# Kernel optimization log

Measured on AMD Instinct MI355X. Metric: run time of the kernel, lower is better.

The kernel has to match this reference:

```python
import jax, jax.numpy as jnp
import numpy as np

NUM_GROUPS = 32
EPS = 1e-05
HT_MIN = -1.0
HT_MAX = 1.0


def setup_inputs() -> dict:
    key = jax.random.key(0)
    k1, k2, k3 = jax.random.split(key, 3)
    B, IN, OUT = 4096, 2048, 2048
    x = jax.random.normal(k1, (B, IN), dtype=jnp.float32)
    # kaiming-uniform-ish scale for weight, uniform bias bound 1/sqrt(in)
    weight = jax.random.normal(k2, (OUT, IN), dtype=jnp.float32) * (1.0 / np.sqrt(IN))
    bias = jax.random.uniform(k3, (OUT,), dtype=jnp.float32, minval=-1.0 / np.sqrt(IN), maxval=1.0 / np.sqrt(IN))
    gn_weight = jnp.ones((OUT,), dtype=jnp.float32)
    gn_bias = jnp.zeros((OUT,), dtype=jnp.float32)
    return {"x": x, "weight": weight, "bias": bias, "gn_weight": gn_weight, "gn_bias": gn_bias}


def reference(x, weight, bias, gn_weight, gn_bias):
    # Linear: y = x @ W^T + b   -> [B, OUT]
    y = jnp.einsum("bi,oi->bo", x, weight) + bias
    B, C = y.shape
    G = NUM_GROUPS
    yg = y.reshape(B, G, C // G)
    mean = jnp.mean(yg, axis=-1, keepdims=True)
    var = jnp.mean(jnp.square(yg), axis=-1, keepdims=True) - jnp.square(mean)
    yn = ((yg - mean) * jax.lax.rsqrt(var + EPS)).reshape(B, C)
    out = yn * gn_weight + gn_bias
    return jnp.clip(out, HT_MIN, HT_MAX)
```

## Files before the change

### kernel.cpp

```cpp
#include <hip/hip_runtime.h>
#include <stdint.h>

#define B_ROWS 4096
#define C_OUT  2048
#define C_IN   2048
#define EPS    1e-5f

typedef __attribute__((ext_vector_type(8))) short bf16x8;
typedef __attribute__((ext_vector_type(4))) float f32x4;

__device__ __forceinline__ unsigned short f2bf(float f) {
    uint32_t u = __float_as_uint(f);
    uint32_t r = (u + 0x7fffu + ((u >> 16) & 1u)) >> 16;
    return (unsigned short)r;
}

__global__ void cvt_f32_bf16_kernel(const float* __restrict__ x,
                                    const float* __restrict__ w,
                                    unsigned short* __restrict__ xb,
                                    unsigned short* __restrict__ wb,
                                    int nx4, int nw4) {
    int i = blockIdx.x * blockDim.x + threadIdx.x;
    const float* src;
    unsigned short* dst;
    if (i < nx4) {
        src = x; dst = xb;
    } else {
        i -= nx4;
        if (i >= nw4) return;
        src = w; dst = wb;
    }
    float4 v = ((const float4*)src)[i];
    ushort4 o;
    o.x = f2bf(v.x); o.y = f2bf(v.y); o.z = f2bf(v.z); o.w = f2bf(v.w);
    ((ushort4*)dst)[i] = o;
}

__global__ __launch_bounds__(512, 2)
void gemm_gn_kernel(const unsigned short* __restrict__ A,
                    const unsigned short* __restrict__ W,
                    const float* __restrict__ bias,
                    const float* __restrict__ gnw,
                    const float* __restrict__ gnb,
                    float* __restrict__ out) {
    __shared__ __align__(16) unsigned short smem[3 * 24576];

    const int bc   = blockIdx.x;
    const int br   = blockIdx.y;
    const int tid  = threadIdx.x;
    const int lane = tid & 63;
    const int wave = tid >> 6;
    const int wr   = wave >> 1;
    const int wc   = wave & 1;
    const int c16  = lane & 15;
    const int quad = lane >> 4;

    f32x4 acc[4][4];
#pragma unroll
    for (int i = 0; i < 4; i++)
#pragma unroll
        for (int j = 0; j < 4; j++) acc[i][j] = (f32x4){0.f, 0.f, 0.f, 0.f};

    const int r0 = tid >> 3;
    const int qo = ((tid & 7) ^ (r0 & 7)) * 8;
    const unsigned short* gA = A + (size_t)(br * 256 + r0) * C_IN + qo;
    const unsigned short* gB = W + (size_t)(bc * 128 + r0) * C_IN + qo;
    const int t8 = tid * 8;

#define STAGE_H(dst, k0, half)                                                                      \
    do {                                                                                            \
        _Pragma("unroll")                                                                           \
        for (int n = (half) * 2; n < (half) * 2 + 2; n++)                                           \
            __builtin_amdgcn_global_load_lds(                                                       \
                (const __attribute__((address_space(1))) void*)(gA + (size_t)(n * 64) * C_IN + (k0)), \
                (__attribute__((address_space(3))) void*)((dst) + n * 4096 + t8), 16, 0, 0);        \
        __builtin_amdgcn_global_load_lds(                                                           \
            (const __attribute__((address_space(1))) void*)(gB + (size_t)((half) * 64) * C_IN + (k0)), \
            (__attribute__((address_space(3))) void*)((dst) + 16384 + (half) * 4096 + t8), 16, 0, 0); \
    } while (0)

    unsigned short* bf0 = smem;
    unsigned short* bf1 = smem + 24576;
    unsigned short* bf2 = smem + 49152;

    const int qs0 = (quad ^ (c16 & 7)) * 8;
    const int qs1 = ((4 + quad) ^ (c16 & 7)) * 8;
    int offA[4], offB[4];
#pragma unroll
    for (int i = 0; i < 4; i++) offA[i] = (wr * 64 + i * 16 + c16) * 64;
#pragma unroll
    for (int j = 0; j < 4; j++) offB[j] = 16384 + (wc * 64 + j * 16 + c16) * 64;

    STAGE_H(bf0, 0, 0);  STAGE_H(bf0, 0, 1);
    STAGE_H(bf1, 64, 0); STAGE_H(bf1, 64, 1);
    asm volatile("s_waitcnt vmcnt(6)" ::: "memory");
    __builtin_amdgcn_s_barrier();

    const unsigned short* pr = bf0;
    const unsigned short* pn = bf1;
    unsigned short*       ps = bf2;

    bf16x8 a0[4], b0[4], a1[4], b1[4];
#pragma unroll
    for (int i = 0; i < 4; i++) a0[i] = *(const bf16x8*)(pr + offA[i] + qs0);
#pragma unroll
    for (int j = 0; j < 4; j++) b0[j] = *(const bf16x8*)(pr + offB[j] + qs0);

#pragma unroll 1
    for (int kt = 0; kt < 32; ++kt) {
        const int k2 = (kt + 2) * 64;

#pragma unroll
        for (int i = 0; i < 4; i++) a1[i] = *(const bf16x8*)(pr + offA[i] + qs1);
#pragma unroll
        for (int j = 0; j < 4; j++) b1[j] = *(const bf16x8*)(pr + offB[j] + qs1);
        if (kt < 30) STAGE_H(ps, k2, 0);
        asm volatile("s_waitcnt lgkmcnt(8)" ::: "memory");
        __builtin_amdgcn_sched_barrier(0);
        __builtin_amdgcn_s_setprio(1);
#pragma unroll
        for (int i = 0; i < 4; i++)
#pragma unroll
            for (int j = 0; j < 4; j++)
                acc[i][j] = __builtin_amdgcn_mfma_f32_16x16x32_bf16(a0[i], b0[j], acc[i][j], 0, 0, 0);
        __builtin_amdgcn_s_setprio(0);

        if (kt < 30)       asm volatile("s_waitcnt vmcnt(3)" ::: "memory");
        else if (kt == 30) asm volatile("s_waitcnt vmcnt(0)" ::: "memory");
        if (kt < 31) {
            __builtin_amdgcn_s_barrier();
#pragma unroll
            for (int i = 0; i < 4; i++) a0[i] = *(const bf16x8*)(pn + offA[i] + qs0);
#pragma unroll
            for (int j = 0; j < 4; j++) b0[j] = *(const bf16x8*)(pn + offB[j] + qs0);
            if (kt < 30) STAGE_H(ps, k2, 1);
            asm volatile("s_waitcnt lgkmcnt(8)" ::: "memory");
        } else {
            asm volatile("s_waitcnt lgkmcnt(0)" ::: "memory");
        }
        __builtin_amdgcn_sched_barrier(0);
        __builtin_amdgcn_s_setprio(1);
#pragma unroll
        for (int i = 0; i < 4; i++)
#pragma unroll
            for (int j = 0; j < 4; j++)
                acc[i][j] = __builtin_amdgcn_mfma_f32_16x16x32_bf16(a1[i], b1[j], acc[i][j], 0, 0, 0);
        __builtin_amdgcn_s_setprio(0);
        if (kt < 31) __builtin_amdgcn_s_barrier();

        const unsigned short* tmp = pr;
        pr = pn;
        pn = ps;
        ps = (unsigned short*)tmp;
    }

    const int colbase = bc * 128 + wc * 64;
    const int rowbase = br * 256 + wr * 64;
    float bv[4], gw[4], gb[4];
#pragma unroll
    for (int j = 0; j < 4; j++) {
        int col = colbase + j * 16 + c16;
        bv[j] = bias[col];
        gw[j] = gnw[col];
        gb[j] = gnb[col];
    }
#pragma unroll
    for (int i = 0; i < 4; i++) {
#pragma unroll
        for (int r = 0; r < 4; r++) {
            float s = 0.f, ss = 0.f;
#pragma unroll
            for (int j = 0; j < 4; j++) {
                float v = acc[i][j][r] + bv[j];
                acc[i][j][r] = v;
                s += v;
                ss += v * v;
            }
#pragma unroll
            for (int m = 1; m < 16; m <<= 1) {
                s  += __shfl_xor(s, m, 64);
                ss += __shfl_xor(ss, m, 64);
            }
            float mean = s * (1.f / 64.f);
            float var  = ss * (1.f / 64.f) - mean * mean;
            float rstd = rsqrtf(var + EPS);
            int row = rowbase + i * 16 + quad * 4 + r;
            float* orow = out + (size_t)row * C_OUT;
#pragma unroll
            for (int j = 0; j < 4; j++) {
                float v = (acc[i][j][r] - mean) * rstd * gw[j] + gb[j];
                v = fminf(1.f, fmaxf(-1.f, v));
                orow[colbase + j * 16 + c16] = v;
            }
        }
    }
}

extern "C" void kernel_launch(void* const* d_in, const int* in_sizes, int n_in,
                              void* d_out, int out_size, void* d_ws, size_t ws_size,
                              hipStream_t stream) {
    const float* x    = (const float*)d_in[0];
    const float* w    = (const float*)d_in[1];
    const float* bias = (const float*)d_in[2];
    const float* gnw  = (const float*)d_in[3];
    const float* gnb  = (const float*)d_in[4];
    float* out = (float*)d_out;

    unsigned short* xb = (unsigned short*)d_ws;
    unsigned short* wb = xb + (size_t)B_ROWS * C_IN;

    const int nx4 = B_ROWS * C_IN / 4;
    const int nw4 = C_OUT * C_IN / 4;
    cvt_f32_bf16_kernel<<<(nx4 + nw4 + 255) / 256, 256, 0, stream>>>(x, w, xb, wb, nx4, nw4);

    dim3 grid(C_OUT / 128, B_ROWS / 256);
    gemm_gn_kernel<<<grid, 512, 0, stream>>>(xb, wb, bias, gnw, gnb, out);
}
```

Baseline: 136.9 us.

## Load A fragments directly to registers, stage only W in LDS, remap blocks to XCDs

```diff
diff --git a/kernel.cpp b/kernel.cpp
--- a/kernel.cpp
+++ b/kernel.cpp
@@ -43,10 +43,14 @@
                     const float* __restrict__ gnw,
                     const float* __restrict__ gnb,
                     float* __restrict__ out) {
-    __shared__ __align__(16) unsigned short smem[3 * 24576];
-
-    const int bc   = blockIdx.x;
-    const int br   = blockIdx.y;
+    __shared__ __align__(16) unsigned short smem[3 * 8192];
+
+    const int bid = blockIdx.x;
+    const int xcd = bid & 7;
+    const int t2  = bid >> 3;
+    const int br  = 2 * xcd + (t2 >> 4);
+    const int bc  = t2 & 15;
+
     const int tid  = threadIdx.x;
     const int lane = tid & 63;
     const int wave = tid >> 6;
@@ -63,80 +67,81 @@
 
     const int r0 = tid >> 3;
     const int qo = ((tid & 7) ^ (r0 & 7)) * 8;
-    const unsigned short* gA = A + (size_t)(br * 256 + r0) * C_IN + qo;
     const unsigned short* gB = W + (size_t)(bc * 128 + r0) * C_IN + qo;
     const int t8 = tid * 8;
 
-#define STAGE_H(dst, k0, half)                                                                      \
-    do {                                                                                            \
-        _Pragma("unroll")                                                                           \
-        for (int n = (half) * 2; n < (half) * 2 + 2; n++)                                           \
-            __builtin_amdgcn_global_load_lds(                                                       \
-                (const __attribute__((address_space(1))) void*)(gA + (size_t)(n * 64) * C_IN + (k0)), \
-                (__attribute__((address_space(3))) void*)((dst) + n * 4096 + t8), 16, 0, 0);        \
-        __builtin_amdgcn_global_load_lds(                                                           \
-            (const __attribute__((address_space(1))) void*)(gB + (size_t)((half) * 64) * C_IN + (k0)), \
-            (__attribute__((address_space(3))) void*)((dst) + 16384 + (half) * 4096 + t8), 16, 0, 0); \
-    } while (0)
+#define STAGE_B(dst, k0, half)                                                                      \
+    __builtin_amdgcn_global_load_lds(                                                               \
+        (const __attribute__((address_space(1))) void*)(gB + (size_t)((half) * 64) * C_IN + (k0)),  \
+        (__attribute__((address_space(3))) void*)((dst) + (half) * 4096 + t8), 16, 0, 0)
 
     unsigned short* bf0 = smem;
-    unsigned short* bf1 = smem + 24576;
-    unsigned short* bf2 = smem + 49152;
+    unsigned short* bf1 = smem + 8192;
+    unsigned short* bf2 = smem + 16384;
 
     const int qs0 = (quad ^ (c16 & 7)) * 8;
     const int qs1 = ((4 + quad) ^ (c16 & 7)) * 8;
-    int offA[4], offB[4];
-#pragma unroll
-    for (int i = 0; i < 4; i++) offA[i] = (wr * 64 + i * 16 + c16) * 64;
-#pragma unroll
-    for (int j = 0; j < 4; j++) offB[j] = 16384 + (wc * 64 + j * 16 + c16) * 64;
-
-    STAGE_H(bf0, 0, 0);  STAGE_H(bf0, 0, 1);
-    STAGE_H(bf1, 64, 0); STAGE_H(bf1, 64, 1);
-    asm volatile("s_waitcnt vmcnt(6)" ::: "memory");
+    int offB[4];
+#pragma unroll
+    for (int j = 0; j < 4; j++) offB[j] = (wc * 64 + j * 16 + c16) * 64;
+
+    const unsigned short* pA[4];
+#pragma unroll
+    for (int i = 0; i < 4; i++)
+        pA[i] = A + (size_t)(br * 256 + wr * 64 + i * 16 + c16) * C_IN + quad * 8;
+
+    STAGE_B(bf0, 0, 0);  STAGE_B(bf0, 0, 1);
+    STAGE_B(bf1, 64, 0); STAGE_B(bf1, 64, 1);
+    bf16x8 ac0[4], ac1[4], an0[4], an1[4], b0[4], b1[4];
+#pragma unroll
+    for (int i = 0; i < 4; i++) ac0[i] = *(const bf16x8*)(pA[i]);
+#pragma unroll
+    for (int i = 0; i < 4; i++) ac1[i] = *(const bf16x8*)(pA[i] + 32);
+    asm volatile("s_waitcnt vmcnt(8)" ::: "memory");
     __builtin_amdgcn_s_barrier();
 
     const unsigned short* pr = bf0;
     const unsigned short* pn = bf1;
     unsigned short*       ps = bf2;
 
-    bf16x8 a0[4], b0[4], a1[4], b1[4];
-#pragma unroll
-    for (int i = 0; i < 4; i++) a0[i] = *(const bf16x8*)(pr + offA[i] + qs0);
 #pragma unroll
     for (int j = 0; j < 4; j++) b0[j] = *(const bf16x8*)(pr + offB[j] + qs0);
 
-#pragma unroll 1
+#pragma unroll 2
     for (int kt = 0; kt < 32; ++kt) {
         const int k2 = (kt + 2) * 64;
 
 #pragma unroll
-        for (int i = 0; i < 4; i++) a1[i] = *(const bf16x8*)(pr + offA[i] + qs1);
-#pragma unroll
         for (int j = 0; j < 4; j++) b1[j] = *(const bf16x8*)(pr + offB[j] + qs1);
-        if (kt < 30) STAGE_H(ps, k2, 0);
-        asm volatile("s_waitcnt lgkmcnt(8)" ::: "memory");
+        __builtin_amdgcn_sched_barrier(0);
+        if (kt < 30) STAGE_B(ps, k2, 0);
+        __builtin_amdgcn_sched_barrier(0);
+        if (kt < 31) {
+#pragma unroll
+            for (int i = 0; i < 4; i++) an0[i] = *(const bf16x8*)(pA[i] + (kt + 1) * 64);
+        }
         __builtin_amdgcn_sched_barrier(0);
         __builtin_amdgcn_s_setprio(1);
 #pragma unroll
         for (int i = 0; i < 4; i++)
 #pragma unroll
             for (int j = 0; j < 4; j++)
-                acc[i][j] = __builtin_amdgcn_mfma_f32_16x16x32_bf16(a0[i], b0[j], acc[i][j], 0, 0, 0);
+                acc[i][j] = __builtin_amdgcn_mfma_f32_16x16x32_bf16(ac0[i], b0[j], acc[i][j], 0, 0, 0);
         __builtin_amdgcn_s_setprio(0);
 
-        if (kt < 30)       asm volatile("s_waitcnt vmcnt(3)" ::: "memory");
-        else if (kt == 30) asm volatile("s_waitcnt vmcnt(0)" ::: "memory");
         if (kt < 31) {
+            if (kt < 30) asm volatile("s_waitcnt vmcnt(9)" ::: "memory");
+            else         asm volatile("s_waitcnt vmcnt(8)" ::: "memory");
             __builtin_amdgcn_s_barrier();
 #pragma unroll
-            for (int i = 0; i < 4; i++) a0[i] = *(const bf16x8*)(pn + offA[i] + qs0);
-#pragma unroll
             for (int j = 0; j < 4; j++) b0[j] = *(const bf16x8*)(pn + offB[j] + qs0);
-            if (kt < 30) STAGE_H(ps, k2, 1);
-            asm volatile("s_waitcnt lgkmcnt(8)" ::: "memory");
-        } else {
-            asm volatile("s_waitcnt lgkmcnt(0)" ::: "memory");
+        }
+        __builtin_amdgcn_sched_barrier(0);
+        if (kt < 30) STAGE_B(ps, k2, 1);
+        __builtin_amdgcn_sched_barrier(0);
+        if (kt < 31) {
+#pragma unroll
+            for (int i = 0; i < 4; i++) an1[i] = *(const bf16x8*)(pA[i] + (kt + 1) * 64 + 32);
         }
         __builtin_amdgcn_sched_barrier(0);
         __builtin_amdgcn_s_setprio(1);
@@ -144,7 +149,7 @@
         for (int i = 0; i < 4; i++)
 #pragma unroll
             for (int j = 0; j < 4; j++)
-                acc[i][j] = __builtin_amdgcn_mfma_f32_16x16x32_bf16(a1[i], b1[j], acc[i][j], 0, 0, 0);
+                acc[i][j] = __builtin_amdgcn_mfma_f32_16x16x32_bf16(ac1[i], b1[j], acc[i][j], 0, 0, 0);
         __builtin_amdgcn_s_setprio(0);
         if (kt < 31) __builtin_amdgcn_s_barrier();
 
@@ -152,6 +157,8 @@
         pr = pn;
         pn = ps;
         ps = (unsigned short*)tmp;
+#pragma unroll
+        for (int i = 0; i < 4; i++) { ac0[i] = an0[i]; ac1[i] = an1[i]; }
     }
 
     const int colbase = bc * 128 + wc * 64;
@@ -213,6 +220,5 @@
     const int nw4 = C_OUT * C_IN / 4;
     cvt_f32_bf16_kernel<<<(nx4 + nw4 + 255) / 256, 256, 0, stream>>>(x, w, xb, wb, nx4, nw4);
 
-    dim3 grid(C_OUT / 128, B_ROWS / 256);
-    gemm_gn_kernel<<<grid, 512, 0, stream>>>(xb, wb, bias, gnw, gnb, out);
-}
+    gemm_gn_kernel<<<256, 512, 0, stream>>>(xb, wb, bias, gnw, gnb, out);
+}
```

Measured after the change: 176.2 us. +28.7%, slower.
